# Kernel optimization log

Hardware: AMD Instinct MI355X
Metric: run time of the kernel (lower is better)

## Reference

```python
import jax, jax.numpy as jnp
import numpy as np
from jax import lax

N_PF = 100
K = 11
F_IN = 36
PDG, FROMPV, PVQ = 0, 1, 2
PX, PY, PZ, EE, VALID = 3, 4, 5, 6, 7
RELETA, RELPHI = 8, 9
F_C = 6 + F_IN - 2          # 40 concat features
ETA_C, PHI_C = RELETA + 4, RELPHI + 4  # positions of rel_eta/rel_phi in concat x
H = 3600
NL = 5
EPS = 1e-3                  # keras BatchNormalization default epsilon
B = 32


def setup_inputs() -> dict:
    key = jax.random.key(0)
    ks = jax.random.split(key, 24)
    xx = jax.random.normal(ks[0], (B, N_PF, F_IN), jnp.float32)
    xx = xx.at[:, :, PDG].set(jax.random.randint(ks[1], (B, N_PF), 0, 350).astype(jnp.float32))
    xx = xx.at[:, :, FROMPV].set(jax.random.randint(ks[2], (B, N_PF), 0, 4).astype(jnp.float32))
    xx = xx.at[:, :, PVQ].set(jax.random.randint(ks[3], (B, N_PF), 0, 8).astype(jnp.float32))
    xx = xx.at[:, :, VALID].set(1.0)
    f32 = jnp.float32
    emb1 = jax.random.normal(ks[4], (350, 2), f32) * 0.05
    emb2 = jax.random.normal(ks[5], (4, 2), f32) * 0.05
    emb3 = jax.random.normal(ks[6], (8, 2), f32) * 0.05
    mean = jax.random.normal(ks[7], (F_IN,), f32) * 0.1
    std = jax.random.uniform(ks[8], (F_IN,), f32, 0.5, 1.5)
    vmin = -jnp.ones((F_IN,), f32) * 3.0
    vmax = jnp.ones((F_IN,), f32) * 3.0
    W0 = jax.random.normal(ks[9], (K * F_C, H), f32) / np.sqrt(K * F_C)
    b0 = jnp.zeros((H,), f32)
    Wh = jax.random.normal(ks[10], (NL - 1, H, H), f32) / np.sqrt(H)
    bh = jnp.zeros((NL - 1, H), f32)
    gamma = jnp.ones((NL, H), f32)
    beta = jnp.zeros((NL, H), f32)
    mmean = jax.random.normal(ks[11], (NL, H), f32) * 0.1
    mvar = jax.random.uniform(ks[12], (NL, H), f32, 0.5, 1.5)
    Wc = jax.random.normal(ks[13], (H, 2), f32) / np.sqrt(H)
    bc = jnp.zeros((2,), f32)
    W2 = jax.random.normal(ks[14], (H, 2), f32) / np.sqrt(H)
    b2 = jnp.zeros((2,), f32)
    W100 = jax.random.normal(ks[15], (H, N_PF), f32) / np.sqrt(H)
    b100 = jnp.zeros((N_PF,), f32)
    return dict(xx=xx, emb1=emb1, emb2=emb2, emb3=emb3, mean=mean, std=std,
                vmin=vmin, vmax=vmax, W0=W0, b0=b0, Wh=Wh, bh=bh, gamma=gamma,
                beta=beta, mmean=mmean, mvar=mvar, Wc=Wc, bc=bc, W2=W2, b2=b2,
                W100=W100, b100=b100)


def reference(xx, emb1, emb2, emb3, mean, std, vmin, vmax, W0, b0, Wh, bh,
              gamma, beta, mmean, mvar, Wc, bc, W2, b2, W100, b100):
    # embeddings on raw (unnormalized) inputs, as in the keras model
    e1 = emb1[jnp.abs(xx[:, :, PDG]).astype(jnp.int32)]
    e2 = emb2[jnp.abs(xx[:, :, FROMPV]).astype(jnp.int32)]
    e3 = emb3[jnp.abs(xx[:, :, PVQ]).astype(jnp.int32)]
    apply_m = jnp.arange(F_IN) >= 3  # id columns not standardized/scaled
    # StdLayer: clip((x-mean)/std, -5, 5)
    y = jnp.clip((xx - mean) / std, -5.0, 5.0)
    x = jnp.where(apply_m, y, xx)
    # ScaleLayer: clip(y*(x-min)+a, a, b) with [a,b]=[-1,1]
    sc = 2.0 / (vmax - vmin)
    y = jnp.clip(sc * (x - vmin) - 1.0, -1.0, 1.0)
    x = jnp.where(apply_m, y, x)
    # concat: [em1, em2, em3, cols 2:]  -> (B, N_PF, F_C)
    x = jnp.concatenate([e1, e2, e3, x[:, :, 2:]], axis=2)
    eta_col = x[:, :, ETA_C]  # (B, N_PF)
    phi_col = x[:, :, PHI_C]

    def bn(h, i):
        return gamma[i] * (h - mmean[i]) * lax.rsqrt(mvar[i] + EPS) + beta[i]

    def mlp(g):  # (B, K*F_C) -> (B, H); dropout is identity at inference
        h = jax.nn.relu(bn(g @ W0 + b0, 0))
        for i in range(1, NL):
            h = jax.nn.relu(bn(h @ Wh[i - 1] + bh[i - 1], i))
        return h

    def knn_step(ref):  # ref: (B, 2) query coordinate
        d = jnp.sqrt(jnp.square(eta_col - ref[:, 0:1]) + jnp.square(phi_col - ref[:, 1:2]))
        _, idx = lax.top_k(-d, K)                              # (B, K)
        g = jnp.take_along_axis(x, idx[:, :, None], axis=1)    # (B, K, F_C)
        h = mlp(g.reshape(g.shape[0], K * F_C))
        return h, h @ Wc + bc

    ref0 = jnp.stack([eta_col[:, 0], phi_col[:, 0]], axis=1)  # anchor = candidate 0
    h, c2 = knn_step(ref0)

    def body(carry, _):
        _, c2 = carry
        return knn_step(c2), None

    (h, c2), _ = lax.scan(body, (h, c2), None, length=N_PF - 1)

    x2 = h @ W2 + b2                                  # (B, 2)
    x100 = jax.nn.softmax(h @ W100 + b100, axis=-1)   # (B, N_PF) per-candidate weights
    w = x100 * xx[:, :, VALID]
    px = jnp.sum(xx[:, :, PX] * w, axis=1)
    py = jnp.sum(xx[:, :, PY] * w, axis=1)
    pz = jnp.sum(xx[:, :, PZ] * w, axis=1)
    E = jnp.sum(xx[:, :, EE] * w, axis=1)
    px2, py2, pz2 = px * px, py * py, pz * pz
    pt = jnp.sqrt(px2 + py2)
    mass2 = E * E - px2 - py2 - pz2                   # model returns m^2 (no sqrt)
    absp = jnp.sqrt(px2 + py2 + pz2)
    cosT = jnp.where(absp == 0, 1.0, pz / jnp.where(absp == 0, 1.0, absp))
    ok = cosT * cosT < 1
    ratio = jnp.where(ok, (1.0 - cosT) / (1.0 + cosT), 1.0)
    eta = jnp.where(ok, -0.5 * jnp.log(ratio), 0.0)
    phi = jnp.where((px == 0) & (py == 0), 0.0, jnp.arctan2(py, px))
    return jnp.stack([x2[:, 0], x2[:, 1], pt, eta, phi, mass2], axis=1)
```

## Files before the change

kernel.cpp:

```cpp
#include <hip/hip_runtime.h>
#include <math.h>

#define NB   32
#define NPF  100
#define FIN  36
#define FC   40
#define KSEL 11
#define HH   3600
#define EPSB 0.001
#define ETA_C 12
#define PHI_C 13
#define MROWS 32
#define PSTRIDE (MROWS * HH)
#define SKH  17
#define KRCH 212
#define SK0  16
#define KRC0 28
#define NJB  29
#define NFIXB 450

__global__ __launch_bounds__(256) void pre_kernel(
    const float* __restrict__ xx, const float* __restrict__ emb1,
    const float* __restrict__ emb2, const float* __restrict__ emb3,
    const float* __restrict__ mean, const float* __restrict__ std_,
    const float* __restrict__ vmin, const float* __restrict__ vmax,
    double* __restrict__ x)
{
    int b = blockIdx.x;
    for (int t = threadIdx.x; t < NPF * FC; t += 256) {
        int p = t / FC, c = t % FC;
        const float* row = xx + (size_t)(b * NPF + p) * FIN;
        double v;
        if (c < 2) {
            int idx = (int)fabsf(row[0]);
            v = (double)emb1[2 * idx + c];
        } else if (c < 4) {
            int idx = (int)fabsf(row[1]);
            v = (double)emb2[2 * idx + (c - 2)];
        } else if (c < 6) {
            int idx = (int)fabsf(row[2]);
            v = (double)emb3[2 * idx + (c - 4)];
        } else {
            int f = c - 4;
            v = (double)row[f];
            if (f >= 3) {
                double y = fmin(fmax((v - (double)mean[f]) / (double)std_[f], -5.0), 5.0);
                double sc = 2.0 / ((double)vmax[f] - (double)vmin[f]);
                v = fmin(fmax(sc * (y - (double)vmin[f]) - 1.0, -1.0), 1.0);
            }
        }
        x[(size_t)(b * NPF + p) * FC + c] = v;
    }
}

__global__ __launch_bounds__(512) void gemm_kernel(
    const double* __restrict__ A, const float* __restrict__ W,
    double* __restrict__ P, int KA, int KRC)
{
    const int tid = threadIdx.x;
    const int rg = __builtin_amdgcn_readfirstlane(tid >> 7);
    const int lh = tid & 127;
    const int j0 = blockIdx.x * 128 + lh;
    const bool jok = (j0 < HH);
    const int jc = jok ? j0 : (HH - 1);
    const int k0 = blockIdx.y * KRC;
    const int kend = min(k0 + KRC, KA);

    double acc[8];
#pragma unroll
    for (int r = 0; r < 8; ++r) acc[r] = 0.0;

    const double* __restrict__ Ap = A + (size_t)k0 * MROWS + rg * 8;
    const float* __restrict__ Wp = W + (size_t)k0 * HH + jc;

#pragma unroll 4
    for (int k = k0; k < kend; ++k) {
        double w0 = (double)(*Wp);
#pragma unroll
        for (int r = 0; r < 8; ++r)
            acc[r] = fma(Ap[r], w0, acc[r]);
        Ap += MROWS;
        Wp += HH;
    }
    if (jok) {
        double* op = P + (size_t)blockIdx.y * PSTRIDE + (size_t)(rg * 8) * HH + j0;
#pragma unroll
        for (int r = 0; r < 8; ++r)
            op[(size_t)r * HH] = acc[r];
    }
}

__global__ __launch_bounds__(256) void fix_kernel(
    const double* __restrict__ P, int nslot,
    const float* __restrict__ bias, const float* __restrict__ gam,
    const float* __restrict__ bet, const float* __restrict__ mm,
    const float* __restrict__ mv, double* __restrict__ Aout,
    const float* __restrict__ Wc, double* __restrict__ c2part, int do_c2)
{
    __shared__ double t[8][33];
    const int tid = threadIdx.x;
    const int r = tid >> 3, jj = tid & 7;
    const int j = blockIdx.x * 8 + jj;
    const double* p = P + (size_t)r * HH + j;
    double s = 0.0;
    for (int sl = 0; sl < nslot; ++sl) s += p[(size_t)sl * PSTRIDE];
    s += (double)bias[j];
    s = (double)gam[j] * (s - (double)mm[j]) * (1.0 / sqrt((double)mv[j] + EPSB))
      + (double)bet[j];
    s = fmax(s, 0.0);
    t[jj][r] = s;
    if (do_c2) {
        double pc0 = s * (double)Wc[2 * j];
        double pc1 = s * (double)Wc[2 * j + 1];
        pc0 += __shfl_xor(pc0, 1); pc1 += __shfl_xor(pc1, 1);
        pc0 += __shfl_xor(pc0, 2); pc1 += __shfl_xor(pc1, 2);
        pc0 += __shfl_xor(pc0, 4); pc1 += __shfl_xor(pc1, 4);
        if (jj == 0) {
            c2part[(size_t)blockIdx.x * 64 + r * 2]     = pc0;
            c2part[(size_t)blockIdx.x * 64 + r * 2 + 1] = pc1;
        }
    }
    __syncthreads();
    const int jj2 = tid >> 5, r2 = tid & 31;
    Aout[(size_t)(blockIdx.x * 8 + jj2) * MROWS + r2] = t[jj2][r2];
}

__global__ __launch_bounds__(256) void knn_kernel(
    const double* __restrict__ x, const double* __restrict__ c2part,
    const float* __restrict__ bc,
    double* __restrict__ g_out, int first)
{
    int b = blockIdx.x, tid = threadIdx.x;
    __shared__ double sd[NPF];
    __shared__ int    sel[KSEL];
    __shared__ double sc2[2];
    __shared__ double red[8];

    double c2x, c2y;
    if (first) {
        c2x = x[(size_t)(b * NPF) * FC + ETA_C];
        c2y = x[(size_t)(b * NPF) * FC + PHI_C];
    } else {
        double ax = 0.0, ay = 0.0;
        for (int blk = tid; blk < NFIXB; blk += 256) {
            ax += c2part[(size_t)blk * 64 + b * 2];
            ay += c2part[(size_t)blk * 64 + b * 2 + 1];
        }
        for (int o = 32; o >= 1; o >>= 1) {
            ax += __shfl_xor(ax, o);
            ay += __shfl_xor(ay, o);
        }
        int wv = tid >> 6;
        if ((tid & 63) == 0) { red[wv * 2] = ax; red[wv * 2 + 1] = ay; }
        __syncthreads();
        if (tid == 0) {
            sc2[0] = red[0] + red[2] + red[4] + red[6] + (double)bc[0];
            sc2[1] = red[1] + red[3] + red[5] + red[7] + (double)bc[1];
        }
        __syncthreads();
        c2x = sc2[0]; c2y = sc2[1];
    }
    if (tid < NPF) {
        double dx = x[(size_t)(b * NPF + tid) * FC + ETA_C] - c2x;
        double dy = x[(size_t)(b * NPF + tid) * FC + PHI_C] - c2y;
        sd[tid] = sqrt(dx * dx + dy * dy);
    }
    __syncthreads();
    if (tid < NPF) {
        double dp = sd[tid];
        int cnt = 0;
        for (int q = 0; q < NPF; ++q) {
            double dq = sd[q];
            cnt += (dq < dp) || (dq == dp && q < tid);
        }
        if (cnt < KSEL) sel[cnt] = tid;
    }
    __syncthreads();
    for (int t = tid; t < KSEL * FC; t += 256) {
        int kk = t / FC, f = t % FC;
        g_out[(size_t)t * MROWS + b] = x[(size_t)(b * NPF + sel[kk]) * FC + f];
    }
}

__global__ __launch_bounds__(256) void head_kernel(
    const float* __restrict__ xx, const double* __restrict__ act,
    const float* __restrict__ W2, const float* __restrict__ b2,
    const float* __restrict__ W100, const float* __restrict__ b100,
    float* __restrict__ out)
{
    int b = blockIdx.x, tid = threadIdx.x;
    __shared__ double hs[HH];
    __shared__ double buf[NPF];
    __shared__ double red[8];
    __shared__ double acc4[4 * NPF];
    __shared__ double sstat[2];

    for (int j = tid; j < HH; j += 256) hs[j] = act[(size_t)j * MROWS + b];
    __syncthreads();
    double a0 = 0.0, a1 = 0.0;
    for (int j = tid; j < HH; j += 256) {
        a0 += hs[j] * (double)W2[2 * j];
        a1 += hs[j] * (double)W2[2 * j + 1];
    }
    for (int o = 32; o >= 1; o >>= 1) { a0 += __shfl_xor(a0, o); a1 += __shfl_xor(a1, o); }
    if ((tid & 63) == 0) { red[(tid >> 6) * 2] = a0; red[(tid >> 6) * 2 + 1] = a1; }
    double lg = 0.0;
    int p = tid >> 1, half = tid & 1;
    if (tid < 2 * NPF) {
        for (int j = half * (HH / 2); j < (half + 1) * (HH / 2); ++j)
            lg += hs[j] * (double)W100[(size_t)j * NPF + p];
    }
    lg += __shfl_xor(lg, 1);
    __syncthreads();
    if (tid < 2 * NPF && half == 0) buf[p] = lg + (double)b100[p];
    __syncthreads();
    if (tid == 0) {
        double m = buf[0];
        for (int q = 1; q < NPF; ++q) m = fmax(m, buf[q]);
        sstat[0] = m;
    }
    __syncthreads();
    if (tid < NPF) buf[tid] = exp(buf[tid] - sstat[0]);
    __syncthreads();
    if (tid == 0) {
        double sm = 0.0;
        for (int q = 0; q < NPF; ++q) sm += buf[q];
        sstat[1] = sm;
    }
    __syncthreads();
    if (tid < NPF) {
        const float* row = xx + (size_t)(b * NPF + tid) * FIN;
        double w = buf[tid] / sstat[1] * (double)row[7];
        acc4[tid]           = (double)row[3] * w;
        acc4[NPF + tid]     = (double)row[4] * w;
        acc4[2 * NPF + tid] = (double)row[5] * w;
        acc4[3 * NPF + tid] = (double)row[6] * w;
    }
    __syncthreads();
    if (tid == 0) {
        double px = 0.0, py = 0.0, pz = 0.0, E = 0.0;
        for (int q = 0; q < NPF; ++q) {
            px += acc4[q]; py += acc4[NPF + q]; pz += acc4[2 * NPF + q]; E += acc4[3 * NPF + q];
        }
        double x2_0 = red[0] + red[2] + red[4] + red[6] + (double)b2[0];
        double x2_1 = red[1] + red[3] + red[5] + red[7] + (double)b2[1];
        double px2 = px * px, py2 = py * py, pz2 = pz * pz;
        double pt = sqrt(px2 + py2);
        double mass2 = E * E - px2 - py2 - pz2;
        double absp = sqrt(px2 + py2 + pz2);
        double cosT = (absp == 0.0) ? 1.0 : pz / absp;
        bool ok = cosT * cosT < 1.0;
        double ratio = ok ? (1.0 - cosT) / (1.0 + cosT) : 1.0;
        double eta = ok ? -0.5 * log(ratio) : 0.0;
        double phi = (px == 0.0 && py == 0.0) ? 0.0 : atan2(py, px);
        out[b * 6 + 0] = (float)x2_0; out[b * 6 + 1] = (float)x2_1; out[b * 6 + 2] = (float)pt;
        out[b * 6 + 3] = (float)eta;  out[b * 6 + 4] = (float)phi;  out[b * 6 + 5] = (float)mass2;
    }
}

extern "C" void kernel_launch(void* const* d_in, const int* in_sizes, int n_in,
                              void* d_out, int out_size, void* d_ws, size_t ws_size,
                              hipStream_t stream)
{
    const float* xx    = (const float*)d_in[0];
    const float* emb1  = (const float*)d_in[1];
    const float* emb2  = (const float*)d_in[2];
    const float* emb3  = (const float*)d_in[3];
    const float* mean  = (const float*)d_in[4];
    const float* std_  = (const float*)d_in[5];
    const float* vmin  = (const float*)d_in[6];
    const float* vmax  = (const float*)d_in[7];
    const float* W0    = (const float*)d_in[8];
    const float* b0    = (const float*)d_in[9];
    const float* Wh    = (const float*)d_in[10];
    const float* bh    = (const float*)d_in[11];
    const float* gamma = (const float*)d_in[12];
    const float* beta  = (const float*)d_in[13];
    const float* mmean = (const float*)d_in[14];
    const float* mvar  = (const float*)d_in[15];
    const float* Wc    = (const float*)d_in[16];
    const float* bc    = (const float*)d_in[17];
    const float* W2    = (const float*)d_in[18];
    const float* b2    = (const float*)d_in[19];
    const float* W100  = (const float*)d_in[20];
    const float* b100  = (const float*)d_in[21];

    double* ws   = (double*)d_ws;
    double* x    = ws;
    double* gbuf = x + NB * NPF * FC;
    double* Aa   = gbuf + 440 * MROWS;
    double* Ab   = Aa + PSTRIDE;
    double* act  = Ab + PSTRIDE;
    double* P    = act + PSTRIDE;
    double* c2part = Ab;

    const size_t HS = (size_t)HH;

    pre_kernel<<<dim3(NB), dim3(256), 0, stream>>>(xx, emb1, emb2, emb3, mean, std_, vmin, vmax, x);

    for (int t = 0; t < NPF; ++t) {
        knn_kernel<<<dim3(NB), dim3(256), 0, stream>>>(x, c2part, bc, gbuf, (t == 0) ? 1 : 0);
        gemm_kernel<<<dim3(NJB, SK0), dim3(512), 0, stream>>>(gbuf, W0, P, 440, KRC0);
        fix_kernel<<<dim3(NFIXB), dim3(256), 0, stream>>>(P, SK0, b0, gamma, beta, mmean, mvar, Aa,
                                                          nullptr, nullptr, 0);
        gemm_kernel<<<dim3(NJB, SKH), dim3(512), 0, stream>>>(Aa, Wh, P, HH, KRCH);
        fix_kernel<<<dim3(NFIXB), dim3(256), 0, stream>>>(P, SKH, bh, gamma + HS, beta + HS,
                                                          mmean + HS, mvar + HS, Ab,
                                                          nullptr, nullptr, 0);
        gemm_kernel<<<dim3(NJB, SKH), dim3(512), 0, stream>>>(Ab, Wh + HS * HS, P, HH, KRCH);
        fix_kernel<<<dim3(NFIXB), dim3(256), 0, stream>>>(P, SKH, bh + HS, gamma + 2 * HS, beta + 2 * HS,
                                                          mmean + 2 * HS, mvar + 2 * HS, Aa,
                                                          nullptr, nullptr, 0);
        gemm_kernel<<<dim3(NJB, SKH), dim3(512), 0, stream>>>(Aa, Wh + 2 * HS * HS, P, HH, KRCH);
        fix_kernel<<<dim3(NFIXB), dim3(256), 0, stream>>>(P, SKH, bh + 2 * HS, gamma + 3 * HS, beta + 3 * HS,
                                                          mmean + 3 * HS, mvar + 3 * HS, Ab,
                                                          nullptr, nullptr, 0);
        gemm_kernel<<<dim3(NJB, SKH), dim3(512), 0, stream>>>(Ab, Wh + 3 * HS * HS, P, HH, KRCH);
        fix_kernel<<<dim3(NFIXB), dim3(256), 0, stream>>>(P, SKH, bh + 3 * HS, gamma + 4 * HS, beta + 4 * HS,
                                                          mmean + 4 * HS, mvar + 4 * HS, act,
                                                          Wc, c2part, 1);
    }
    head_kernel<<<dim3(NB), dim3(256), 0, stream>>>(xx, act, W2, b2, W100, b100, (float*)d_out);
}
```

Baseline: 17.85 ms.

## Stage W tiles in double-buffered LDS and compute two columns per thread

The fp64 GEMM kernel now loads 32-row by 256-column tiles of the float weight matrix into shared memory with coalesced float4 loads. The next tile is prefetched into registers while the current one is used, then written to the other buffer. Each thread now accumulates two adjacent output columns, so each A value is reused for two FMAs, and results are stored as double2. This removes strided scalar W loads and halves A traffic per output, at the cost of more LDS, more registers and half as many column blocks.

```diff
diff --git a/kernel.cpp b/kernel.cpp
--- a/kernel.cpp
+++ b/kernel.cpp
@@ -16,7 +16,9 @@
 #define KRCH 212
 #define SK0  16
 #define KRC0 28
-#define NJB  29
+#define NJB  15
+#define JB   256
+#define TK   32
 #define NFIXB 450
 
 __global__ __launch_bounds__(256) void pre_kernel(
@@ -57,36 +59,93 @@
     const double* __restrict__ A, const float* __restrict__ W,
     double* __restrict__ P, int KA, int KRC)
 {
+    __shared__ float wt[2][TK][JB];
+
     const int tid = threadIdx.x;
     const int rg = __builtin_amdgcn_readfirstlane(tid >> 7);
     const int lh = tid & 127;
-    const int j0 = blockIdx.x * 128 + lh;
+    const int jbase = blockIdx.x * JB;
+    const int j0 = jbase + lh * 2;
     const bool jok = (j0 < HH);
-    const int jc = jok ? j0 : (HH - 1);
     const int k0 = blockIdx.y * KRC;
     const int kend = min(k0 + KRC, KA);
-
-    double acc[8];
-#pragma unroll
-    for (int r = 0; r < 8; ++r) acc[r] = 0.0;
-
-    const double* __restrict__ Ap = A + (size_t)k0 * MROWS + rg * 8;
-    const float* __restrict__ Wp = W + (size_t)k0 * HH + jc;
-
+    const int nch = (kend - k0 + TK - 1) / TK;
+
+    const int maxcf = HH - jbase - 4;
+    int srow[4], scol[4];
+#pragma unroll
+    for (int q = 0; q < 4; ++q) {
+        int f = q * 512 + tid;
+        srow[q] = f >> 6;
+        scol[q] = min((f & 63) * 4, maxcf);
+    }
+
+    double acc[8][2];
+#pragma unroll
+    for (int r = 0; r < 8; ++r) { acc[r][0] = 0.0; acc[r][1] = 0.0; }
+
+    float4 stg[4];
+#pragma unroll
+    for (int q = 0; q < 4; ++q) {
+        int krow = min(k0 + srow[q], KA - 1);
+        stg[q] = *(const float4*)(W + (size_t)krow * HH + jbase + scol[q]);
+    }
+#pragma unroll
+    for (int q = 0; q < 4; ++q)
+        *(float4*)&wt[0][srow[q]][scol[q]] = stg[q];
+
+    int cur = 0;
+    for (int c = 0; c < nch; ++c) {
+        const int kc = k0 + c * TK;
+        const int len = min(TK, kend - kc);
+        const bool more = (c + 1 < nch);
+
+        if (more) {
+            const int kb = kc + TK;
+#pragma unroll
+            for (int q = 0; q < 4; ++q) {
+                int krow = min(kb + srow[q], KA - 1);
+                stg[q] = *(const float4*)(W + (size_t)krow * HH + jbase + scol[q]);
+            }
+        }
+        __syncthreads();
+
+        const double* __restrict__ Apc = A + (size_t)kc * MROWS + rg * 8;
+        const float* __restrict__ wrow = &wt[cur][0][lh * 2];
+
+#define GSTEP(kk)                                                     \
+        {                                                             \
+            float2 wv = *(const float2*)(wrow + (kk) * JB);           \
+            double w0 = (double)wv.x, w1 = (double)wv.y;              \
+            _Pragma("unroll")                                         \
+            for (int r = 0; r < 8; ++r) {                             \
+                double a = Apc[(kk) * MROWS + r];                     \
+                acc[r][0] = fma(a, w0, acc[r][0]);                    \
+                acc[r][1] = fma(a, w1, acc[r][1]);                    \
+            }                                                         \
+        }
+        if (len == TK) {
 #pragma unroll 4
-    for (int k = k0; k < kend; ++k) {
-        double w0 = (double)(*Wp);
-#pragma unroll
-        for (int r = 0; r < 8; ++r)
-            acc[r] = fma(Ap[r], w0, acc[r]);
-        Ap += MROWS;
-        Wp += HH;
-    }
+            for (int kk = 0; kk < TK; ++kk) GSTEP(kk)
+        } else {
+#pragma unroll 4
+            for (int kk = 0; kk < len; ++kk) GSTEP(kk)
+        }
+#undef GSTEP
+
+        if (more) {
+#pragma unroll
+            for (int q = 0; q < 4; ++q)
+                *(float4*)&wt[cur ^ 1][srow[q]][scol[q]] = stg[q];
+        }
+        cur ^= 1;
+    }
+
     if (jok) {
         double* op = P + (size_t)blockIdx.y * PSTRIDE + (size_t)(rg * 8) * HH + j0;
 #pragma unroll
         for (int r = 0; r < 8; ++r)
-            op[(size_t)r * HH] = acc[r];
+            *(double2*)(op + (size_t)r * HH) = make_double2(acc[r][0], acc[r][1]);
     }
 }
 
```

Result: slower. 23.65 ms (+32.5%).
